# Kernel optimization log

Measured on AMD Instinct MI355X. Metric: run time of the kernel, lower is better.

## Reference

```python
import jax, jax.numpy as jnp
import numpy as np

# Cyclic permutation matrices applied after each flow step (dimension==3 branch)
P_XY = jnp.array([[0, 1, 0], [1, 0, 0], [0, 0, 1]], dtype=jnp.float32)
P_XZ = jnp.array([[0, 0, 1], [0, 1, 0], [1, 0, 0]], dtype=jnp.float32)
P_YZ = jnp.array([[0, 1, 0], [0, 0, 1], [1, 0, 0]], dtype=jnp.float32)

N = 1_000_000   # number of atoms / samples
FLOW_DEPTH = 8


def setup_inputs() -> dict:
    key = jax.random.key(0)
    k1, k2, k3 = jax.random.split(key, 3)
    z = jax.random.normal(k1, (N, 3), dtype=jnp.float32)
    w = jax.random.normal(k2, (N, FLOW_DEPTH, 3, 3), dtype=jnp.float32)
    b = jax.random.normal(k3, (N, FLOW_DEPTH, 3), dtype=jnp.float32)
    return {"z": z, "w": w, "b": b}


def _flow_zx(z, w, b):
    # z: [N,3], w: [N,D,3,3], b: [N,D,3]
    eye = jnp.eye(3, dtype=w.dtype)
    diag = jnp.diagonal(w, axis1=-2, axis2=-1)               # [N,D,3]
    # LU parameterization: unit lower-tri L, positive diag D, unit upper-tri U
    l = jnp.tril(w, -1) + eye
    u = jnp.triu(w, 1) + eye
    # Faithful to original: log-det uses |0.1 + diag|, D uses |diag| + 0.1
    d_log_det = jnp.sum(jnp.log(jnp.abs(0.1 + diag)), axis=(1, 2))  # [N]
    du = (jnp.abs(diag) + 0.1)[..., :, None] * u             # D @ U, [N,D,3,3]
    W = jnp.einsum('ndij,ndjk->ndik', l, du)                  # L @ D @ U
    perms = [P_XY, P_YZ, P_XZ]
    depth = w.shape[1]
    for idx in range(depth):  # static, small flow depth
        z = jnp.einsum('nb,nbd->nd', z, W[:, idx]) + b[:, idx]
        z = z @ perms[idx % 3]
    return z, d_log_det


def reference(z, w, b):
    return _flow_zx(z, w, b)
```

## Files before the change

kernel.cpp:

```cpp
#include <hip/hip_runtime.h>

#define FLOW_DEPTH 8
#define BLOCK 64
#define W_F4 18
#define B_F4 6
#define CH   65

typedef const __attribute__((address_space(1))) void g_void;
typedef __attribute__((address_space(3))) void l_void;

__global__ __launch_bounds__(BLOCK) void graphflow_kernel(
    const float* __restrict__ z_in,
    const float* __restrict__ w,
    const float* __restrict__ b,
    float* __restrict__ out,
    int n_atoms)
{
    __shared__ float4 sw[(W_F4 - 1) * CH + BLOCK];

    const int t = threadIdx.x;
    const int atom0 = blockIdx.x * BLOCK;
    const int n = atom0 + t;

    const float4* gw = reinterpret_cast<const float4*>(w) + (size_t)atom0 * W_F4;
    const bool full = (atom0 + BLOCK <= n_atoms);

    if (full) {
#pragma unroll
        for (int k = 0; k < W_F4; ++k) {
            __builtin_amdgcn_global_load_lds((g_void*)(gw + k * BLOCK + t),
                                             (l_void*)(sw + k * CH), 16, 0, 0);
        }
    } else {
        int nw = (n_atoms - atom0) * W_F4;
        for (int k = 0; k < W_F4; ++k) {
            int idx = k * BLOCK + t;
            if (idx < nw) sw[idx + (idx >> 6)] = gw[idx];
        }
        __syncthreads();
    }

    float4 br[B_F4];
    float z0 = 0.f, z1 = 0.f, z2 = 0.f;
    if (n < n_atoms) {
        const float4* gb = reinterpret_cast<const float4*>(b) + (size_t)n * B_F4;
#pragma unroll
        for (int j = 0; j < B_F4; ++j) br[j] = gb[j];
        z0 = z_in[n * 3 + 0];
        z1 = z_in[n * 3 + 1];
        z2 = z_in[n * 3 + 2];
    }

    __builtin_amdgcn_s_waitcnt(0);

    if (n >= n_atoms) return;

    float4 wr[W_F4];
#pragma unroll
    for (int j = 0; j < W_F4; ++j) {
        int i = t * W_F4 + j;
        wr[j] = sw[i + (i >> 6)];
    }

    const float* wf = reinterpret_cast<const float*>(wr);
    const float* bf = reinterpret_cast<const float*>(br);

    float logdet = 0.0f;

#pragma unroll
    for (int d = 0; d < FLOW_DEPTH; ++d) {
        const float* W = wf + d * 9;
        float w00 = W[0], w01 = W[1], w02 = W[2];
        float w10 = W[3], w11 = W[4], w12 = W[5];
        float w20 = W[6], w21 = W[7], w22 = W[8];

        float d0 = fabsf(w00) + 0.1f;
        float d1 = fabsf(w11) + 0.1f;
        float d2 = fabsf(w22) + 0.1f;
        logdet += __logf(fabsf((0.1f + w00) * (0.1f + w11) * (0.1f + w22)));

        float m01 = d0 * w01;
        float m02 = d0 * w02;
        float m12 = d1 * w12;
        float M00 = d0;
        float M01 = m01;
        float M02 = m02;
        float M10 = w10 * d0;
        float M11 = fmaf(w10, m01, d1);
        float M12 = fmaf(w10, m02, m12);
        float M20 = w20 * d0;
        float M21 = fmaf(w20, m01, w21 * d1);
        float M22 = fmaf(w20, m02, fmaf(w21, m12, d2));

        float t0 = fmaf(z0, M00, fmaf(z1, M10, fmaf(z2, M20, bf[d * 3 + 0])));
        float t1 = fmaf(z0, M01, fmaf(z1, M11, fmaf(z2, M21, bf[d * 3 + 1])));
        float t2 = fmaf(z0, M02, fmaf(z1, M12, fmaf(z2, M22, bf[d * 3 + 2])));

        int p = d % 3;
        if (p == 0) {
            z0 = t1; z1 = t0; z2 = t2;
        } else if (p == 1) {
            z0 = t2; z1 = t0; z2 = t1;
        } else {
            z0 = t2; z1 = t1; z2 = t0;
        }
    }

    out[n * 3 + 0] = z0;
    out[n * 3 + 1] = z1;
    out[n * 3 + 2] = z2;
    out[(size_t)3 * n_atoms + n] = logdet;
}

extern "C" void kernel_launch(void* const* d_in, const int* in_sizes, int n_in,
                              void* d_out, int out_size, void* d_ws, size_t ws_size,
                              hipStream_t stream) {
    const float* z = (const float*)d_in[0];
    const float* w = (const float*)d_in[1];
    const float* b = (const float*)d_in[2];
    float* out = (float*)d_out;

    int n_atoms = in_sizes[0] / 3;
    int grid = (n_atoms + BLOCK - 1) / BLOCK;

    hipLaunchKernelGGL(graphflow_kernel, dim3(grid), dim3(BLOCK), 0, stream,
                       z, w, b, out, n_atoms);
}
```

Baseline: 444.2 us.

## Convert to persistent grid with double-buffered LDS prefetch of next tile

Replaces one-block-per-tile launch with a persistent grid of 1024 blocks that loop over tiles, double-buffering the weight tile in LDS via async global_load_lds and prefetching the next tile's z and b into registers while computing the current one. The goal is to overlap memory latency with compute and cut per-block launch and drain overhead. It adds a partial vmcnt wait and more registers, and a grid of 1024 single-wave blocks may not expose enough memory parallelism to saturate HBM bandwidth. Partial tiles fall back to direct global loads.

```diff
diff --git a/kernel.cpp b/kernel.cpp
--- a/kernel.cpp
+++ b/kernel.cpp
@@ -1,115 +1,144 @@
 #include <hip/hip_runtime.h>
 
 #define FLOW_DEPTH 8
-#define BLOCK 64
+#define TILE 64
 #define W_F4 18
 #define B_F4 6
 #define CH   65
+#define GRID 1024
 
 typedef const __attribute__((address_space(1))) void g_void;
 typedef __attribute__((address_space(3))) void l_void;
 
-__global__ __launch_bounds__(BLOCK) void graphflow_kernel(
+#define WAIT_VM(n) __builtin_amdgcn_s_waitcnt((((n) & 0xF) | ((((n) >> 4) & 0x3) << 14) | (0x7 << 4) | (0xF << 8)))
+
+__global__ __launch_bounds__(TILE) void graphflow_kernel(
     const float* __restrict__ z_in,
     const float* __restrict__ w,
     const float* __restrict__ b,
     float* __restrict__ out,
     int n_atoms)
 {
-    __shared__ float4 sw[(W_F4 - 1) * CH + BLOCK];
+    __shared__ float4 sw[2][W_F4 * CH];
 
     const int t = threadIdx.x;
-    const int atom0 = blockIdx.x * BLOCK;
-    const int n = atom0 + t;
+    const int n_tiles = (n_atoms + TILE - 1) / TILE;
+    int tile = blockIdx.x;
+    if (tile >= n_tiles) return;
 
-    const float4* gw = reinterpret_cast<const float4*>(w) + (size_t)atom0 * W_F4;
-    const bool full = (atom0 + BLOCK <= n_atoms);
+    auto issue_dma = [&](int tl, int bf) {
+        const float4* gw = reinterpret_cast<const float4*>(w) + (size_t)tl * (TILE * W_F4);
+#pragma unroll
+        for (int k = 0; k < W_F4; ++k)
+            __builtin_amdgcn_global_load_lds((g_void*)(gw + k * TILE + t),
+                                             (l_void*)(&sw[bf][k * CH]), 16, 0, 0);
+    };
+    auto load_zb = [&](int tl, float4* brr, float& a0, float& a1, float& a2) {
+        int a = tl * TILE + t;
+        if (a < n_atoms) {
+            const float4* gb = reinterpret_cast<const float4*>(b) + (size_t)a * B_F4;
+#pragma unroll
+            for (int j = 0; j < B_F4; ++j) brr[j] = gb[j];
+            a0 = z_in[a * 3 + 0];
+            a1 = z_in[a * 3 + 1];
+            a2 = z_in[a * 3 + 2];
+        }
+    };
 
-    if (full) {
+    bool cur_full = (tile * TILE + TILE <= n_atoms);
+    float4 br_c[B_F4];
+    float zc0 = 0.f, zc1 = 0.f, zc2 = 0.f;
+    load_zb(tile, br_c, zc0, zc1, zc2);
+    if (cur_full) issue_dma(tile, 0);
+
+    int buf = 0;
+    for (;;) {
+        const int nxt = tile + GRID;
+        const bool has_next = (nxt < n_tiles);
+        const bool nxt_full = has_next && (nxt * TILE + TILE <= n_atoms);
+
+        float4 br_n[B_F4];
+        float zn0 = 0.f, zn1 = 0.f, zn2 = 0.f;
+        if (has_next) load_zb(nxt, br_n, zn0, zn1, zn2);
+        if (nxt_full) issue_dma(nxt, buf ^ 1);
+
+        if (nxt_full) WAIT_VM(18); else WAIT_VM(0);
+        __builtin_amdgcn_sched_barrier(0);
+
+        const int a = tile * TILE + t;
+        if (a < n_atoms) {
+            float4 wr[W_F4];
+            if (cur_full) {
 #pragma unroll
-        for (int k = 0; k < W_F4; ++k) {
-            __builtin_amdgcn_global_load_lds((g_void*)(gw + k * BLOCK + t),
-                                             (l_void*)(sw + k * CH), 16, 0, 0);
-        }
-    } else {
-        int nw = (n_atoms - atom0) * W_F4;
-        for (int k = 0; k < W_F4; ++k) {
-            int idx = k * BLOCK + t;
-            if (idx < nw) sw[idx + (idx >> 6)] = gw[idx];
-        }
-        __syncthreads();
-    }
+                for (int j = 0; j < W_F4; ++j) {
+                    int i = t * W_F4 + j;
+                    wr[j] = sw[buf][i + (i >> 6)];
+                }
+            } else {
+                const float4* gwa = reinterpret_cast<const float4*>(w) + (size_t)a * W_F4;
+#pragma unroll
+                for (int j = 0; j < W_F4; ++j) wr[j] = gwa[j];
+            }
 
-    float4 br[B_F4];
-    float z0 = 0.f, z1 = 0.f, z2 = 0.f;
-    if (n < n_atoms) {
-        const float4* gb = reinterpret_cast<const float4*>(b) + (size_t)n * B_F4;
-#pragma unroll
-        for (int j = 0; j < B_F4; ++j) br[j] = gb[j];
-        z0 = z_in[n * 3 + 0];
-        z1 = z_in[n * 3 + 1];
-        z2 = z_in[n * 3 + 2];
-    }
+            const float* wf = reinterpret_cast<const float*>(wr);
+            const float* bf2 = reinterpret_cast<const float*>(br_c);
 
-    __builtin_amdgcn_s_waitcnt(0);
-
-    if (n >= n_atoms) return;
-
-    float4 wr[W_F4];
-#pragma unroll
-    for (int j = 0; j < W_F4; ++j) {
-        int i = t * W_F4 + j;
-        wr[j] = sw[i + (i >> 6)];
-    }
-
-    const float* wf = reinterpret_cast<const float*>(wr);
-    const float* bf = reinterpret_cast<const float*>(br);
-
-    float logdet = 0.0f;
+            float z0 = zc0, z1 = zc1, z2 = zc2;
+            float logdet = 0.0f;
 
 #pragma unroll
-    for (int d = 0; d < FLOW_DEPTH; ++d) {
-        const float* W = wf + d * 9;
-        float w00 = W[0], w01 = W[1], w02 = W[2];
-        float w10 = W[3], w11 = W[4], w12 = W[5];
-        float w20 = W[6], w21 = W[7], w22 = W[8];
+            for (int d = 0; d < FLOW_DEPTH; ++d) {
+                const float* W = wf + d * 9;
+                float w00 = W[0], w01 = W[1], w02 = W[2];
+                float w10 = W[3], w11 = W[4], w12 = W[5];
+                float w20 = W[6], w21 = W[7], w22 = W[8];
 
-        float d0 = fabsf(w00) + 0.1f;
-        float d1 = fabsf(w11) + 0.1f;
-        float d2 = fabsf(w22) + 0.1f;
-        logdet += __logf(fabsf((0.1f + w00) * (0.1f + w11) * (0.1f + w22)));
+                float d0 = fabsf(w00) + 0.1f;
+                float d1 = fabsf(w11) + 0.1f;
+                float d2 = fabsf(w22) + 0.1f;
+                logdet += __logf(fabsf((0.1f + w00) * (0.1f + w11) * (0.1f + w22)));
 
-        float m01 = d0 * w01;
-        float m02 = d0 * w02;
-        float m12 = d1 * w12;
-        float M00 = d0;
-        float M01 = m01;
-        float M02 = m02;
-        float M10 = w10 * d0;
-        float M11 = fmaf(w10, m01, d1);
-        float M12 = fmaf(w10, m02, m12);
-        float M20 = w20 * d0;
-        float M21 = fmaf(w20, m01, w21 * d1);
-        float M22 = fmaf(w20, m02, fmaf(w21, m12, d2));
+                float m01 = d0 * w01;
+                float m02 = d0 * w02;
+                float m12 = d1 * w12;
+                float M00 = d0;
+                float M01 = m01;
+                float M02 = m02;
+                float M10 = w10 * d0;
+                float M11 = fmaf(w10, m01, d1);
+                float M12 = fmaf(w10, m02, m12);
+                float M20 = w20 * d0;
+                float M21 = fmaf(w20, m01, w21 * d1);
+                float M22 = fmaf(w20, m02, fmaf(w21, m12, d2));
 
-        float t0 = fmaf(z0, M00, fmaf(z1, M10, fmaf(z2, M20, bf[d * 3 + 0])));
-        float t1 = fmaf(z0, M01, fmaf(z1, M11, fmaf(z2, M21, bf[d * 3 + 1])));
-        float t2 = fmaf(z0, M02, fmaf(z1, M12, fmaf(z2, M22, bf[d * 3 + 2])));
+                float t0 = fmaf(z0, M00, fmaf(z1, M10, fmaf(z2, M20, bf2[d * 3 + 0])));
+                float t1 = fmaf(z0, M01, fmaf(z1, M11, fmaf(z2, M21, bf2[d * 3 + 1])));
+                float t2 = fmaf(z0, M02, fmaf(z1, M12, fmaf(z2, M22, bf2[d * 3 + 2])));
 
-        int p = d % 3;
-        if (p == 0) {
-            z0 = t1; z1 = t0; z2 = t2;
-        } else if (p == 1) {
-            z0 = t2; z1 = t0; z2 = t1;
-        } else {
-            z0 = t2; z1 = t1; z2 = t0;
+                int p = d % 3;
+                if (p == 0) {
+                    z0 = t1; z1 = t0; z2 = t2;
+                } else if (p == 1) {
+                    z0 = t2; z1 = t0; z2 = t1;
+                } else {
+                    z0 = t2; z1 = t1; z2 = t0;
+                }
+            }
+
+            out[a * 3 + 0] = z0;
+            out[a * 3 + 1] = z1;
+            out[a * 3 + 2] = z2;
+            out[(size_t)3 * n_atoms + a] = logdet;
         }
+
+        if (!has_next) break;
+        tile = nxt;
+        cur_full = nxt_full;
+        buf ^= 1;
+#pragma unroll
+        for (int j = 0; j < B_F4; ++j) br_c[j] = br_n[j];
+        zc0 = zn0; zc1 = zn1; zc2 = zn2;
     }
-
-    out[n * 3 + 0] = z0;
-    out[n * 3 + 1] = z1;
-    out[n * 3 + 2] = z2;
-    out[(size_t)3 * n_atoms + n] = logdet;
 }
 
 extern "C" void kernel_launch(void* const* d_in, const int* in_sizes, int n_in,
@@ -121,8 +150,9 @@
     float* out = (float*)d_out;
 
     int n_atoms = in_sizes[0] / 3;
-    int grid = (n_atoms + BLOCK - 1) / BLOCK;
+    int n_tiles = (n_atoms + TILE - 1) / TILE;
+    int grid = n_tiles < GRID ? n_tiles : GRID;
 
-    hipLaunchKernelGGL(graphflow_kernel, dim3(grid), dim3(BLOCK), 0, stream,
+    hipLaunchKernelGGL(graphflow_kernel, dim3(grid), dim3(TILE), 0, stream,
                        z, w, b, out, n_atoms);
 }
```

After: 450.5 us. No clear change (+1.4%).
